# Kernel tuning notes

Measured on AMD Instinct MI355X. Metric: run time of the kernel, lower is better.

## Reference

```python
import jax, jax.numpy as jnp
import numpy as np

B, S, HID, NH = 1, 2048, 4096, 32
D = HID // NH            # head_dim = 128
HP = NH // 2             # 16 differential head-pairs
DEPTH = 1
LAMBDA_INIT = 0.8 - 0.6 * float(np.exp(-0.3 * DEPTH))
EPS = 1e-5


def setup_inputs() -> dict:
    key = jax.random.key(0)
    ks = jax.random.split(key, 9)
    s = 0.02
    return {
        "hidden_states": jax.random.normal(ks[0], (B, S, HID), jnp.float32),
        "Wqkv_w": jax.random.normal(ks[1], (3 * HID, HID), jnp.float32) * s,
        "Wqkv_b": jnp.zeros((3 * HID,), jnp.float32),
        "out_w": jax.random.normal(ks[2], (HID, HID), jnp.float32) * s,
        "out_b": jnp.zeros((HID,), jnp.float32),
        "lambda_q1": jax.random.normal(ks[3], (D,), jnp.float32) * 0.1,
        "lambda_k1": jax.random.normal(ks[4], (D,), jnp.float32) * 0.1,
        "lambda_q2": jax.random.normal(ks[5], (D,), jnp.float32) * 0.1,
        "lambda_k2": jax.random.normal(ks[6], (D,), jnp.float32) * 0.1,
        "subln_w": jnp.ones((2 * D,), jnp.float32),
    }


def _rmsnorm(x, w):
    xf = x.astype(jnp.float32)
    var = jnp.mean(xf * xf, axis=-1, keepdims=True)
    return (w * (xf * jax.lax.rsqrt(var + EPS))).astype(x.dtype)


def reference(hidden_states, Wqkv_w, Wqkv_b, out_w, out_b,
              lambda_q1, lambda_k1, lambda_q2, lambda_k2, subln_w):
    # QKV projection: op_size = H*D + 2*(Hkv*D) with Hkv == H
    qkv = hidden_states @ Wqkv_w.T + Wqkv_b          # [B,S,3*HID]
    q, k, v = jnp.split(qkv, 3, axis=-1)
    # split_heads: heads laid out as (H_pair, two, D)
    q = q.reshape(B, S, HP, 2, D)
    k = k.reshape(B, S, HP, 2, D)
    v12 = v.reshape(B, S, HP, 2 * D)                 # concat(v1, v2) along feature dim
    q1, q2 = q[..., 0, :], q[..., 1, :]
    k1, k2 = k[..., 0, :], k[..., 1, :]

    scale = D ** -0.5
    causal = jnp.tril(jnp.ones((S, S), bool))        # [S,S]

    def attend(qi, ki):
        # attn(qi,ki,v1) cat attn(qi,ki,v2) == softmax(qi ki^T) @ [v1;v2]
        sc = jnp.einsum('bqhd,bkhd->bhqk', qi, ki) * scale
        sc = jnp.where(causal, sc, -1e30)
        p = jax.nn.softmax(sc, axis=-1)
        return jnp.einsum('bhqk,bkhe->bqhe', p, v12)  # [B,S,HP,2D]

    attn1 = attend(q1, k1)
    attn2 = attend(q2, k2)

    lam1 = jnp.exp(jnp.sum(lambda_q1 * lambda_k1))
    lam2 = jnp.exp(jnp.sum(lambda_q2 * lambda_k2))
    lambda_full = lam1 - lam2 + LAMBDA_INIT

    attn = attn1 - lambda_full * attn2
    attn = _rmsnorm(attn, subln_w) * (1.0 - LAMBDA_INIT)
    # '... H (two D) -> ... (H two) D' then merge heads -> [B,S,HID]
    attn = attn.reshape(B, S, HID)
    return attn @ out_w.T + out_b
```

## Files before the change

kernel.cpp:

```cpp
#include <hip/hip_runtime.h>
#include <stdint.h>

#define LAMBDA_INIT_F 0.35550906759096927f
#define ONE_MINUS_LI_F 0.6444909324090307f
#define QSCALE_F 0.08838834764831845f

typedef __attribute__((ext_vector_type(8))) short bf16x8;
typedef __attribute__((ext_vector_type(4))) float f32x4;

__device__ __forceinline__ unsigned short f2bf(float x) {
    union { float f; uint32_t u; } v; v.f = x;
    uint32_t r = v.u + 0x7fffu + ((v.u >> 16) & 1u);
    return (unsigned short)(r >> 16);
}
__device__ __forceinline__ float bf2f(unsigned short h) {
    union { uint32_t u; float f; } v; v.u = ((uint32_t)h) << 16;
    return v.f;
}
__device__ __forceinline__ f32x4 mfma16(bf16x8 a, bf16x8 b, f32x4 c) {
    return __builtin_amdgcn_mfma_f32_16x16x32_bf16(a, b, c, 0, 0, 0);
}
__device__ __forceinline__ void split_store8(float4 a, float4 b,
                                             unsigned short* dh, unsigned short* dl) {
    union { unsigned short u[8]; bf16x8 v; } H, L;
    float f[8] = {a.x, a.y, a.z, a.w, b.x, b.y, b.z, b.w};
    #pragma unroll
    for (int e = 0; e < 8; ++e) {
        unsigned short hh = f2bf(f[e]);
        H.u[e] = hh;
        L.u[e] = f2bf(f[e] - bf2f(hh));
    }
    *(bf16x8*)dh = H.v;
    *(bf16x8*)dl = L.v;
}

template<int MODE>
__global__ __launch_bounds__(256, 2) void gemm_split_kernel(
    const float* __restrict__ A, const float* __restrict__ Bm,
    const float* __restrict__ bias, int M, int N, int K,
    unsigned short* __restrict__ qh, unsigned short* __restrict__ ql,
    unsigned short* __restrict__ kh, unsigned short* __restrict__ kl,
    unsigned short* __restrict__ vh, unsigned short* __restrict__ vl,
    float* __restrict__ Cout)
{
    __shared__ unsigned short sAh[128 * 72], sAl[128 * 72];
    __shared__ unsigned short sBh[128 * 72], sBl[128 * 72];

    const int nwg = gridDim.x;
    const int bid = blockIdx.x;
    const int wg  = (bid & 7) * (nwg >> 3) + (bid >> 3);
    const int mt  = M >> 7;
    const int bm  = wg % mt, bn = wg / mt;
    const int rowA = bm << 7, rowB = bn << 7;

    const int t  = threadIdx.x;
    const int g  = t & 7, mr = t >> 3;
    const int ln = t & 63, w = t >> 6;
    const int wm = (w >> 1) << 6, wn = (w & 1) << 6;
    const int lr = ln & 15, lg = ln >> 4;

    const f32x4 zero4 = {0.f, 0.f, 0.f, 0.f};
    f32x4 acc[4][4];
    #pragma unroll
    for (int a = 0; a < 4; ++a)
        #pragma unroll
        for (int b = 0; b < 4; ++b) acc[a][b] = zero4;

    for (int k0 = 0; k0 < K; k0 += 64) {
        float4 st[16];
        #pragma unroll
        for (int i = 0; i < 4; ++i) {
            const float* sa = A  + (size_t)(rowA + mr + 32 * i) * K + k0 + g * 8;
            const float* sb = Bm + (size_t)(rowB + mr + 32 * i) * K + k0 + g * 8;
            st[2 * i]     = *(const float4*)sa;
            st[2 * i + 1] = *(const float4*)(sa + 4);
            st[8 + 2 * i]     = *(const float4*)sb;
            st[8 + 2 * i + 1] = *(const float4*)(sb + 4);
        }
        #pragma unroll
        for (int i = 0; i < 4; ++i) {
            const int off = (mr + 32 * i) * 72 + g * 8;
            split_store8(st[2 * i],     st[2 * i + 1],     &sAh[off], &sAl[off]);
            split_store8(st[8 + 2 * i], st[8 + 2 * i + 1], &sBh[off], &sBl[off]);
        }
        __syncthreads();

        #pragma unroll
        for (int kk = 0; kk < 2; ++kk) {
            bf16x8 ah[4], al_[4], bh[4], bl_[4];
            const int ko = kk * 32 + lg * 8;
            #pragma unroll
            for (int mf = 0; mf < 4; ++mf) {
                const int off = (wm + mf * 16 + lr) * 72 + ko;
                ah[mf]  = *(const bf16x8*)&sAh[off];
                al_[mf] = *(const bf16x8*)&sAl[off];
            }
            #pragma unroll
            for (int nf = 0; nf < 4; ++nf) {
                const int off = (wn + nf * 16 + lr) * 72 + ko;
                bh[nf]  = *(const bf16x8*)&sBh[off];
                bl_[nf] = *(const bf16x8*)&sBl[off];
            }
            #pragma unroll
            for (int mf = 0; mf < 4; ++mf)
                #pragma unroll
                for (int nf = 0; nf < 4; ++nf) {
                    acc[mf][nf] = mfma16(ah[mf],  bh[nf],  acc[mf][nf]);
                    acc[mf][nf] = mfma16(ah[mf],  bl_[nf], acc[mf][nf]);
                    acc[mf][nf] = mfma16(al_[mf], bh[nf],  acc[mf][nf]);
                }
        }
        __syncthreads();
    }

    #pragma unroll
    for (int nf = 0; nf < 4; ++nf) {
        const int n  = (bn << 7) + wn + nf * 16 + lr;
        const float bv = bias[n];
        #pragma unroll
        for (int mf = 0; mf < 4; ++mf) {
            #pragma unroll
            for (int i = 0; i < 4; ++i) {
                const int srow = (bm << 7) + wm + mf * 16 + lg * 4 + i;
                const float val = acc[mf][nf][i] + bv;
                if (MODE == 0) {
                    if (n < 4096) {
                        const int hh = n >> 8, e2 = (n >> 7) & 1, d = n & 127;
                        const float qv = val * QSCALE_F;
                        const unsigned short hi = f2bf(qv);
                        const unsigned short lo = f2bf(qv - bf2f(hi));
                        const size_t o = ((size_t)((hh * 2 + e2) * 2048 + srow)) * 128 + d;
                        qh[o] = hi; ql[o] = lo;
                    } else if (n < 8192) {
                        const int n2 = n - 4096;
                        const int hh = n2 >> 8, e2 = (n2 >> 7) & 1, d = n2 & 127;
                        const unsigned short hi = f2bf(val);
                        const unsigned short lo = f2bf(val - bf2f(hi));
                        const size_t o = ((size_t)((hh * 2 + e2) * 2048 + srow)) * 128 + d;
                        kh[o] = hi; kl[o] = lo;
                    } else {
                        const int n2 = n - 8192;
                        const int hh = n2 >> 8, cc = n2 & 255;
                        const unsigned short hi = f2bf(val);
                        const unsigned short lo = f2bf(val - bf2f(hi));
                        const size_t o = ((size_t)(hh * 256 + cc)) * 2048 + srow;
                        vh[o] = hi; vl[o] = lo;
                    }
                } else {
                    Cout[(size_t)srow * N + n] = val;
                }
            }
        }
    }
}

__global__ __launch_bounds__(512, 2) void attn_kernel(
    const unsigned short* __restrict__ qh, const unsigned short* __restrict__ ql,
    const unsigned short* __restrict__ kh, const unsigned short* __restrict__ kl,
    const unsigned short* __restrict__ vh, const unsigned short* __restrict__ vl,
    float* __restrict__ att1, float* __restrict__ att2)
{
    __shared__ unsigned short sK[2][2][32 * 136];
    __shared__ unsigned short sV[2][256 * 40];
    __shared__ unsigned short sP[8][2][16 * 40];

    const int qt = blockIdx.x;
    const int h  = blockIdx.y;
    const int t  = threadIdx.x;
    const int w  = t >> 6, ln = t & 63;
    const int e  = w >> 2, wq = w & 3;
    const int lr = ln & 15, lg = ln >> 4;
    const int qr0 = qt * 64 + wq * 16;

    bf16x8 qfh[4], qfl[4];
    {
        const size_t qoff = ((size_t)((h * 2 + e) * 2048 + qr0 + lr)) * 128 + lg * 8;
        #pragma unroll
        for (int kk = 0; kk < 4; ++kk) {
            qfh[kk] = *(const bf16x8*)(qh + qoff + kk * 32);
            qfl[kk] = *(const bf16x8*)(ql + qoff + kk * 32);
        }
    }

    const f32x4 zero4 = {0.f, 0.f, 0.f, 0.f};
    f32x4 o[16];
    #pragma unroll
    for (int nf = 0; nf < 16; ++nf) o[nf] = zero4;
    float mrun[4] = {-3.0e38f, -3.0e38f, -3.0e38f, -3.0e38f};
    float lrun[4] = {0.f, 0.f, 0.f, 0.f};

    const int ktiles = qt * 2 + 2;
    for (int kt = 0; kt < ktiles; ++kt) {
        bf16x8 stg[8];
        unsigned short* dstp[8];
        #pragma unroll
        for (int i = 0; i < 8; ++i) {
            const int gid = i * 512 + t;
            if (gid < 2048) {
                const int buf = gid >> 9, r = gid & 511;
                const int e2 = buf >> 1, hl = buf & 1;
                const int key = r >> 4, dg = r & 15;
                const unsigned short* base = hl ? kl : kh;
                stg[i]  = *(const bf16x8*)(base +
                          ((size_t)((h * 2 + e2) * 2048 + kt * 32 + key)) * 128 + dg * 8);
                dstp[i] = &sK[e2][hl][key * 136 + dg * 8];
            } else {
                const int r2 = gid - 2048;
                const int hl = r2 >> 10, r = r2 & 1023;
                const int c = r >> 2, kg = r & 3;
                const unsigned short* base = hl ? vl : vh;
                stg[i]  = *(const bf16x8*)(base +
                          ((size_t)(h * 256 + c)) * 2048 + kt * 32 + kg * 8);
                dstp[i] = &sV[hl][c * 40 + kg * 8];
            }
        }
        #pragma unroll
        for (int i = 0; i < 8; ++i) *(bf16x8*)dstp[i] = stg[i];
        __syncthreads();

        f32x4 s[2];
        s[0] = zero4; s[1] = zero4;
        #pragma unroll
        for (int kk = 0; kk < 4; ++kk) {
            const int ko = kk * 32 + lg * 8;
            #pragma unroll
            for (int nf = 0; nf < 2; ++nf) {
                const int off = (nf * 16 + lr) * 136 + ko;
                const bf16x8 kbh = *(const bf16x8*)&sK[e][0][off];
                const bf16x8 kbl = *(const bf16x8*)&sK[e][1][off];
                s[nf] = mfma16(qfh[kk], kbh, s[nf]);
                s[nf] = mfma16(qfh[kk], kbl, s[nf]);
                s[nf] = mfma16(qfl[kk], kbh, s[nf]);
            }
        }

        const int key0 = kt * 32 + lr;
        #pragma unroll
        for (int i = 0; i < 4; ++i) {
            const int qrow = qr0 + lg * 4 + i;
            float s0 = s[0][i], s1 = s[1][i];
            if (key0 > qrow)      s0 = -1e30f;
            if (key0 + 16 > qrow) s1 = -1e30f;
            float r = fmaxf(s0, s1);
            r = fmaxf(r, __shfl_xor(r, 1));
            r = fmaxf(r, __shfl_xor(r, 2));
            r = fmaxf(r, __shfl_xor(r, 4));
            r = fmaxf(r, __shfl_xor(r, 8));
            const float mnew = fmaxf(mrun[i], r);
            const float corr = expf(mrun[i] - mnew);
            const float p0 = expf(s0 - mnew);
            const float p1 = expf(s1 - mnew);
            float rs = p0 + p1;
            rs += __shfl_xor(rs, 1); rs += __shfl_xor(rs, 2);
            rs += __shfl_xor(rs, 4); rs += __shfl_xor(rs, 8);
            lrun[i] = lrun[i] * corr + rs;
            mrun[i] = mnew;
            const int prow = (lg * 4 + i) * 40;
            const unsigned short h0 = f2bf(p0);
            sP[w][0][prow + lr]      = h0;
            sP[w][1][prow + lr]      = f2bf(p0 - bf2f(h0));
            const unsigned short h1 = f2bf(p1);
            sP[w][0][prow + 16 + lr] = h1;
            sP[w][1][prow + 16 + lr] = f2bf(p1 - bf2f(h1));
            #pragma unroll
            for (int nf = 0; nf < 16; ++nf) o[nf][i] *= corr;
        }

        const int poff = lr * 40 + lg * 8;
        const bf16x8 ph  = *(const bf16x8*)&sP[w][0][poff];
        const bf16x8 pl_ = *(const bf16x8*)&sP[w][1][poff];
        #pragma unroll
        for (int nf = 0; nf < 16; ++nf) {
            const int voff = (nf * 16 + lr) * 40 + lg * 8;
            const bf16x8 vbh = *(const bf16x8*)&sV[0][voff];
            const bf16x8 vbl = *(const bf16x8*)&sV[1][voff];
            o[nf] = mfma16(ph,  vbh, o[nf]);
            o[nf] = mfma16(ph,  vbl, o[nf]);
            o[nf] = mfma16(pl_, vbh, o[nf]);
        }
        __syncthreads();
    }

    float* dst = e ? att2 : att1;
    #pragma unroll
    for (int i = 0; i < 4; ++i) {
        const float inv = 1.0f / lrun[i];
        const int srow = qr0 + lg * 4 + i;
        float* p = dst + ((size_t)srow * 16 + h) * 256 + lr;
        #pragma unroll
        for (int nf = 0; nf < 16; ++nf) p[nf * 16] = o[nf][i] * inv;
    }
}

__global__ __launch_bounds__(256, 4) void combine_kernel(
    const float* __restrict__ att1, const float* __restrict__ att2,
    const float* __restrict__ lq1, const float* __restrict__ lk1,
    const float* __restrict__ lq2, const float* __restrict__ lk2,
    const float* __restrict__ slnw, float* __restrict__ attn_f)
{
    const int t = threadIdx.x, w = t >> 6, ln = t & 63;
    const int idx = blockIdx.x * 4 + w;

    float d1 = lq1[ln] * lk1[ln] + lq1[ln + 64] * lk1[ln + 64];
    float d2 = lq2[ln] * lk2[ln] + lq2[ln + 64] * lk2[ln + 64];
    #pragma unroll
    for (int off = 1; off < 64; off <<= 1) {
        d1 += __shfl_xor(d1, off);
        d2 += __shfl_xor(d2, off);
    }
    const float lamf = expf(d1) - expf(d2) + LAMBDA_INIT_F;

    const size_t base = (size_t)idx * 256 + ln * 4;
    const float4 x1 = *(const float4*)(att1 + base);
    const float4 x2 = *(const float4*)(att2 + base);
    float x[4] = { x1.x - lamf * x2.x, x1.y - lamf * x2.y,
                   x1.z - lamf * x2.z, x1.w - lamf * x2.w };
    float ss = x[0] * x[0] + x[1] * x[1] + x[2] * x[2] + x[3] * x[3];
    #pragma unroll
    for (int off = 1; off < 64; off <<= 1) ss += __shfl_xor(ss, off);
    const float sc = ONE_MINUS_LI_F / sqrtf(ss * (1.0f / 256.0f) + 1e-5f);
    const float4 wv = *(const float4*)(slnw + ln * 4);
    float4 y;
    y.x = x[0] * sc * wv.x; y.y = x[1] * sc * wv.y;
    y.z = x[2] * sc * wv.z; y.w = x[3] * sc * wv.w;
    *(float4*)(attn_f + base) = y;
}

extern "C" void kernel_launch(void* const* d_in, const int* in_sizes, int n_in,
                              void* d_out, int out_size, void* d_ws, size_t ws_size,
                              hipStream_t stream)
{
    const float* hs   = (const float*)d_in[0];
    const float* wqkv = (const float*)d_in[1];
    const float* bqkv = (const float*)d_in[2];
    const float* wout = (const float*)d_in[3];
    const float* bout = (const float*)d_in[4];
    const float* lq1  = (const float*)d_in[5];
    const float* lk1  = (const float*)d_in[6];
    const float* lq2  = (const float*)d_in[7];
    const float* lk2  = (const float*)d_in[8];
    const float* slnw = (const float*)d_in[9];

    uint8_t* ws = (uint8_t*)d_ws;
    const size_t NQ = (size_t)16 * 2 * 2048 * 128;
    unsigned short* qh_ = (unsigned short*)(ws);
    unsigned short* ql_ = (unsigned short*)(ws + NQ * 2);
    unsigned short* kh_ = (unsigned short*)(ws + NQ * 4);
    unsigned short* kl_ = (unsigned short*)(ws + NQ * 6);
    unsigned short* vh_ = (unsigned short*)(ws + NQ * 8);
    unsigned short* vl_ = (unsigned short*)(ws + NQ * 10);
    float* att2  = (float*)(ws + NQ * 12);
    float* attnf = (float*)(ws + NQ * 12 + NQ * 4);
    float* att1  = (float*)d_out;

    gemm_split_kernel<0><<<1536, 256, 0, stream>>>(hs, wqkv, bqkv, 2048, 12288, 4096,
        qh_, ql_, kh_, kl_, vh_, vl_, nullptr);
    attn_kernel<<<dim3(32, 16), 512, 0, stream>>>(qh_, ql_, kh_, kl_, vh_, vl_, att1, att2);
    combine_kernel<<<8192, 256, 0, stream>>>(att1, att2, lq1, lk1, lq2, lk2, slnw, attnf);
    gemm_split_kernel<1><<<512, 256, 0, stream>>>(attnf, wout, bout, 2048, 4096, 4096,
        nullptr, nullptr, nullptr, nullptr, nullptr, nullptr, (float*)d_out);
}
```

Before: 2.217 ms.

## Pre-split fp32 operands to bf16 hi/lo and use direct-to-LDS loads in GEMMs

Adds a standalone kernel that splits fp32 activations and weights into bf16 hi/lo planes ahead of time. A new GEMM then streams those planes straight into LDS with global_load_lds, using an XOR-swizzled layout, so the per-tile fp32-to-bf16 split disappears from the inner loop. The QKV weight is split and multiplied in six column chunks so it fits the workspace, and the combine kernel writes its output already split. This costs extra launches and extra global traffic for the split copies, and it only runs when the workspace is large enough.

```diff
diff --git a/kernel.cpp b/kernel.cpp
--- a/kernel.cpp
+++ b/kernel.cpp
@@ -8,20 +8,20 @@
 typedef __attribute__((ext_vector_type(8))) short bf16x8;
 typedef __attribute__((ext_vector_type(4))) float f32x4;
 
-__device__ __forceinline__ unsigned short f2bf(float x) {
+static __device__ __forceinline__ unsigned short f2bf(float x) {
     union { float f; uint32_t u; } v; v.f = x;
     uint32_t r = v.u + 0x7fffu + ((v.u >> 16) & 1u);
     return (unsigned short)(r >> 16);
 }
-__device__ __forceinline__ float bf2f(unsigned short h) {
+static __device__ __forceinline__ float bf2f(unsigned short h) {
     union { uint32_t u; float f; } v; v.u = ((uint32_t)h) << 16;
     return v.f;
 }
-__device__ __forceinline__ f32x4 mfma16(bf16x8 a, bf16x8 b, f32x4 c) {
+static __device__ __forceinline__ f32x4 mfma16(bf16x8 a, bf16x8 b, f32x4 c) {
     return __builtin_amdgcn_mfma_f32_16x16x32_bf16(a, b, c, 0, 0, 0);
 }
-__device__ __forceinline__ void split_store8(float4 a, float4 b,
-                                             unsigned short* dh, unsigned short* dl) {
+static __device__ __forceinline__ void split_store8(float4 a, float4 b,
+                                                    unsigned short* dh, unsigned short* dl) {
     union { unsigned short u[8]; bf16x8 v; } H, L;
     float f[8] = {a.x, a.y, a.z, a.w, b.x, b.y, b.z, b.w};
     #pragma unroll
@@ -32,6 +32,143 @@
     }
     *(bf16x8*)dh = H.v;
     *(bf16x8*)dl = L.v;
+}
+static __device__ __forceinline__ void gload_lds16(const unsigned short* g, unsigned short* l) {
+    __builtin_amdgcn_global_load_lds(
+        (const __attribute__((address_space(1))) void*)g,
+        (__attribute__((address_space(3))) void*)l, 16, 0, 0);
+}
+
+__global__ __launch_bounds__(256) void split_fp32_kernel(
+    const float* __restrict__ src,
+    unsigned short* __restrict__ hi, unsigned short* __restrict__ lo, int n8)
+{
+    const int i = blockIdx.x * 256 + threadIdx.x;
+    if (i >= n8) return;
+    const float4 a = ((const float4*)src)[2 * i];
+    const float4 b = ((const float4*)src)[2 * i + 1];
+    split_store8(a, b, hi + (size_t)i * 8, lo + (size_t)i * 8);
+}
+
+template<int MODE>
+__global__ __launch_bounds__(256, 3) void gemm_bs_kernel(
+    const unsigned short* __restrict__ Ah, const unsigned short* __restrict__ Al,
+    const unsigned short* __restrict__ Bh, const unsigned short* __restrict__ Bl,
+    const float* __restrict__ bias, int M, int Nc, int K, int n0, int Nfull,
+    unsigned short* __restrict__ qh, unsigned short* __restrict__ ql,
+    unsigned short* __restrict__ kh, unsigned short* __restrict__ kl,
+    unsigned short* __restrict__ vh, unsigned short* __restrict__ vl,
+    float* __restrict__ Cout)
+{
+    __shared__ __attribute__((aligned(16))) unsigned short sA[128 * 64];
+    __shared__ __attribute__((aligned(16))) unsigned short sB[128 * 64];
+
+    const int nwg = gridDim.x;
+    const int bid = blockIdx.x;
+    const int wg  = (bid & 7) * (nwg >> 3) + (bid >> 3);
+    const int mt  = M >> 7;
+    const int bm  = wg % mt, bn = wg / mt;
+    const int rowA = bm << 7, rowB = bn << 7;
+
+    const int t = threadIdx.x, ln = t & 63, w = t >> 6;
+    const int wm = (w >> 1) << 6, wn = (w & 1) << 6;
+    const int lr = ln & 15, lg = ln >> 4;
+
+    const int r8 = ln >> 3, p = ln & 7;
+    const int sl = p ^ r8;
+    const unsigned short* pA = (sl < 4) ? Ah : Al;
+    const unsigned short* pB = (sl < 4) ? Bh : Bl;
+    const int co = (sl & 3) << 3;
+    const unsigned short* baseA[4];
+    const unsigned short* baseB[4];
+    unsigned short* ldsA[4];
+    unsigned short* ldsB[4];
+    #pragma unroll
+    for (int i = 0; i < 4; ++i) {
+        const int r = (w << 5) + i * 8;
+        baseA[i] = pA + (size_t)(rowA + r + r8) * K + co;
+        baseB[i] = pB + (size_t)(rowB + r + r8) * K + co;
+        ldsA[i]  = &sA[r << 6];
+        ldsB[i]  = &sB[r << 6];
+    }
+
+    const f32x4 zero4 = {0.f, 0.f, 0.f, 0.f};
+    f32x4 acc[4][4];
+    #pragma unroll
+    for (int a = 0; a < 4; ++a)
+        #pragma unroll
+        for (int b = 0; b < 4; ++b) acc[a][b] = zero4;
+
+    for (int k0 = 0; k0 < K; k0 += 32) {
+        #pragma unroll
+        for (int i = 0; i < 4; ++i) {
+            gload_lds16(baseA[i] + k0, ldsA[i]);
+            gload_lds16(baseB[i] + k0, ldsB[i]);
+        }
+        __syncthreads();
+
+        const int so = (lg ^ (lr & 7)) << 3;
+        bf16x8 ah[4], al_[4];
+        #pragma unroll
+        for (int mf = 0; mf < 4; ++mf) {
+            const int ar = (wm + mf * 16 + lr) << 6;
+            ah[mf]  = *(const bf16x8*)&sA[ar + so];
+            al_[mf] = *(const bf16x8*)&sA[ar + (so ^ 32)];
+        }
+        #pragma unroll
+        for (int nf = 0; nf < 4; ++nf) {
+            const int br = (wn + nf * 16 + lr) << 6;
+            const bf16x8 bh  = *(const bf16x8*)&sB[br + so];
+            const bf16x8 bl_ = *(const bf16x8*)&sB[br + (so ^ 32)];
+            #pragma unroll
+            for (int mf = 0; mf < 4; ++mf) {
+                acc[mf][nf] = mfma16(ah[mf],  bh,  acc[mf][nf]);
+                acc[mf][nf] = mfma16(ah[mf],  bl_, acc[mf][nf]);
+                acc[mf][nf] = mfma16(al_[mf], bh,  acc[mf][nf]);
+            }
+        }
+        __syncthreads();
+    }
+
+    #pragma unroll
+    for (int nf = 0; nf < 4; ++nf) {
+        const int n  = n0 + (bn << 7) + wn + nf * 16 + lr;
+        const float bv = bias[n];
+        #pragma unroll
+        for (int mf = 0; mf < 4; ++mf) {
+            #pragma unroll
+            for (int i = 0; i < 4; ++i) {
+                const int srow = (bm << 7) + wm + mf * 16 + lg * 4 + i;
+                const float val = acc[mf][nf][i] + bv;
+                if (MODE == 0) {
+                    if (n < 4096) {
+                        const int hh = n >> 8, e2 = (n >> 7) & 1, d = n & 127;
+                        const float qv = val * QSCALE_F;
+                        const unsigned short hi = f2bf(qv);
+                        const unsigned short lo = f2bf(qv - bf2f(hi));
+                        const size_t o = ((size_t)((hh * 2 + e2) * 2048 + srow)) * 128 + d;
+                        qh[o] = hi; ql[o] = lo;
+                    } else if (n < 8192) {
+                        const int n2 = n - 4096;
+                        const int hh = n2 >> 8, e2 = (n2 >> 7) & 1, d = n2 & 127;
+                        const unsigned short hi = f2bf(val);
+                        const unsigned short lo = f2bf(val - bf2f(hi));
+                        const size_t o = ((size_t)((hh * 2 + e2) * 2048 + srow)) * 128 + d;
+                        kh[o] = hi; kl[o] = lo;
+                    } else {
+                        const int n2 = n - 8192;
+                        const int hh = n2 >> 8, cc = n2 & 255;
+                        const unsigned short hi = f2bf(val);
+                        const unsigned short lo = f2bf(val - bf2f(hi));
+                        const size_t o = ((size_t)(hh * 256 + cc)) * 2048 + srow;
+                        vh[o] = hi; vl[o] = lo;
+                    }
+                } else {
+                    Cout[(size_t)srow * Nfull + n] = val;
+                }
+            }
+        }
+    }
 }
 
 template<int MODE>
@@ -292,11 +429,13 @@
     }
 }
 
+template<int SPLITOUT>
 __global__ __launch_bounds__(256, 4) void combine_kernel(
     const float* __restrict__ att1, const float* __restrict__ att2,
     const float* __restrict__ lq1, const float* __restrict__ lk1,
     const float* __restrict__ lq2, const float* __restrict__ lk2,
-    const float* __restrict__ slnw, float* __restrict__ attn_f)
+    const float* __restrict__ slnw, float* __restrict__ attn_f,
+    unsigned short* __restrict__ aoh, unsigned short* __restrict__ aol)
 {
     const int t = threadIdx.x, w = t >> 6, ln = t & 63;
     const int idx = blockIdx.x * 4 + w;
@@ -320,10 +459,21 @@
     for (int off = 1; off < 64; off <<= 1) ss += __shfl_xor(ss, off);
     const float sc = ONE_MINUS_LI_F / sqrtf(ss * (1.0f / 256.0f) + 1e-5f);
     const float4 wv = *(const float4*)(slnw + ln * 4);
-    float4 y;
-    y.x = x[0] * sc * wv.x; y.y = x[1] * sc * wv.y;
-    y.z = x[2] * sc * wv.z; y.w = x[3] * sc * wv.w;
-    *(float4*)(attn_f + base) = y;
+    float y[4] = { x[0] * sc * wv.x, x[1] * sc * wv.y,
+                   x[2] * sc * wv.z, x[3] * sc * wv.w };
+    if (SPLITOUT) {
+        union { unsigned short u[4]; uint64_t q; } H, L;
+        #pragma unroll
+        for (int j = 0; j < 4; ++j) {
+            H.u[j] = f2bf(y[j]);
+            L.u[j] = f2bf(y[j] - bf2f(H.u[j]));
+        }
+        *(uint64_t*)(aoh + base) = H.q;
+        *(uint64_t*)(aol + base) = L.q;
+    } else {
+        float4 yv = { y[0], y[1], y[2], y[3] };
+        *(float4*)(attn_f + base) = yv;
+    }
 }
 
 extern "C" void kernel_launch(void* const* d_in, const int* in_sizes, int n_in,
@@ -343,20 +493,52 @@
 
     uint8_t* ws = (uint8_t*)d_ws;
     const size_t NQ = (size_t)16 * 2 * 2048 * 128;
+    const size_t PL = NQ * 2;
     unsigned short* qh_ = (unsigned short*)(ws);
-    unsigned short* ql_ = (unsigned short*)(ws + NQ * 2);
-    unsigned short* kh_ = (unsigned short*)(ws + NQ * 4);
-    unsigned short* kl_ = (unsigned short*)(ws + NQ * 6);
-    unsigned short* vh_ = (unsigned short*)(ws + NQ * 8);
-    unsigned short* vl_ = (unsigned short*)(ws + NQ * 10);
-    float* att2  = (float*)(ws + NQ * 12);
-    float* attnf = (float*)(ws + NQ * 12 + NQ * 4);
-    float* att1  = (float*)d_out;
-
-    gemm_split_kernel<0><<<1536, 256, 0, stream>>>(hs, wqkv, bqkv, 2048, 12288, 4096,
-        qh_, ql_, kh_, kl_, vh_, vl_, nullptr);
-    attn_kernel<<<dim3(32, 16), 512, 0, stream>>>(qh_, ql_, kh_, kl_, vh_, vl_, att1, att2);
-    combine_kernel<<<8192, 256, 0, stream>>>(att1, att2, lq1, lk1, lq2, lk2, slnw, attnf);
-    gemm_split_kernel<1><<<512, 256, 0, stream>>>(attnf, wout, bout, 2048, 4096, 4096,
-        nullptr, nullptr, nullptr, nullptr, nullptr, nullptr, (float*)d_out);
-}
+    unsigned short* ql_ = (unsigned short*)(ws + PL);
+    unsigned short* kh_ = (unsigned short*)(ws + 2 * PL);
+    unsigned short* kl_ = (unsigned short*)(ws + 3 * PL);
+    unsigned short* vh_ = (unsigned short*)(ws + 4 * PL);
+    unsigned short* vl_ = (unsigned short*)(ws + 5 * PL);
+    float* att1 = (float*)d_out;
+    float* att2 = (float*)(ws + 6 * PL);
+
+    const size_t NEED = 167772160ull;
+    if (ws_size >= NEED) {
+        unsigned short* Hsh = (unsigned short*)(ws + 6 * PL);
+        unsigned short* Hsl = (unsigned short*)(ws + 7 * PL);
+        unsigned short* Wbh = (unsigned short*)(ws + 8 * PL);
+        unsigned short* Wbl = (unsigned short*)(ws + 9 * PL);
+        unsigned short* Aoh = (unsigned short*)(ws);
+        unsigned short* Aol = (unsigned short*)(ws + PL);
+        unsigned short* Oh  = (unsigned short*)(ws + 2 * PL);
+        unsigned short* Ol  = (unsigned short*)(ws + 4 * PL);
+
+        split_fp32_kernel<<<4096, 256, 0, stream>>>(hs, Hsh, Hsl, 1048576);
+        for (int c = 0; c < 6; ++c) {
+            split_fp32_kernel<<<4096, 256, 0, stream>>>(
+                wqkv + (size_t)c * 2048 * 4096, Wbh, Wbl, 1048576);
+            gemm_bs_kernel<0><<<256, 256, 0, stream>>>(Hsh, Hsl, Wbh, Wbl, bqkv,
+                2048, 2048, 4096, c * 2048, 12288,
+                qh_, ql_, kh_, kl_, vh_, vl_, nullptr);
+        }
+        attn_kernel<<<dim3(32, 16), 512, 0, stream>>>(qh_, ql_, kh_, kl_, vh_, vl_,
+                                                      att1, att2);
+        combine_kernel<1><<<8192, 256, 0, stream>>>(att1, att2, lq1, lk1, lq2, lk2, slnw,
+            nullptr, Aoh, Aol);
+        split_fp32_kernel<<<8192, 256, 0, stream>>>(wout, Oh, Ol, 2097152);
+        gemm_bs_kernel<1><<<512, 256, 0, stream>>>(Aoh, Aol, Oh, Ol, bout,
+            2048, 4096, 4096, 0, 4096,
+            nullptr, nullptr, nullptr, nullptr, nullptr, nullptr, (float*)d_out);
+    } else {
+        float* attnf = (float*)(ws + 6 * PL + NQ * 4);
+        gemm_split_kernel<0><<<1536, 256, 0, stream>>>(hs, wqkv, bqkv, 2048, 12288, 4096,
+            qh_, ql_, kh_, kl_, vh_, vl_, nullptr);
+        attn_kernel<<<dim3(32, 16), 512, 0, stream>>>(qh_, ql_, kh_, kl_, vh_, vl_,
+                                                      att1, att2);
+        combine_kernel<0><<<8192, 256, 0, stream>>>(att1, att2, lq1, lk1, lq2, lk2, slnw,
+            attnf, nullptr, nullptr);
+        gemm_split_kernel<1><<<512, 256, 0, stream>>>(attnf, wout, bout, 2048, 4096, 4096,
+            nullptr, nullptr, nullptr, nullptr, nullptr, nullptr, (float*)d_out);
+    }
+}
```

Measured after the change: 1.987 ms. 1.12x faster.
